# Kernel tuning notes

Hardware: AMD Instinct MI355X
Metric: run time of the kernel (lower is better)

Reference implementation:

```python
import jax, jax.numpy as jnp
import numpy as np

N, E, D, C = 50000, 800000, 96, 40
L2_EPS = 1e-12  # tf.nn.l2_normalize epsilon


def setup_inputs() -> dict:
    key = jax.random.key(0)
    ks = jax.random.split(key, 8)
    row = jnp.sort(jax.random.randint(ks[0], (E,), 0, N, dtype=jnp.int32))
    col = jax.random.randint(ks[1], (E,), 0, N, dtype=jnp.int32)
    vals = jax.random.uniform(ks[2], (E,), dtype=jnp.float32)
    x = jax.random.normal(ks[3], (N, D), dtype=jnp.float32)
    w1 = jax.random.normal(ks[4], (D, D), dtype=jnp.float32) * 0.1
    w2 = jax.random.normal(ks[5], (D, D), dtype=jnp.float32) * 0.1
    wc = jax.random.normal(ks[6], (D, C), dtype=jnp.float32) * 0.1
    bc = jnp.zeros((C,), dtype=jnp.float32)
    return {"row": row, "col": col, "vals": vals, "x": x,
            "w1": w1, "w2": w2, "wc": wc, "bc": bc}


def _spmm(row, col, vals, h):
    # sparse A (coo: row, col, vals) @ dense h, via gather + segment_sum
    msg = vals[:, None] * h[col]            # [E, D]
    return jax.ops.segment_sum(msg, row, num_segments=N)


def reference(row, col, vals, x, w1, w2, wc, bc):
    h = x
    for w in (w1, w2):                       # GCNConv: act(A @ (h @ W)), no bias
        h = jax.nn.relu(_spmm(row, col, vals, h @ w))
    # tf.nn.l2_normalize(h, axis=1)
    sq = jnp.sum(h * h, axis=1, keepdims=True)
    out = h * jax.lax.rsqrt(jnp.maximum(sq, L2_EPS))
    probs = jax.nn.softmax(out @ wc + bc, axis=-1)
    return out, probs
```

## Files before the change

### kernel.cpp

```cpp
#include <hip/hip_runtime.h>
#include <hip/hip_bf16.h>

#define GN 50000
#define GE 800000
#define GD 96
#define GC 40
#define L2EPS 1e-12f

typedef __attribute__((ext_vector_type(8))) short short8v;
typedef __attribute__((ext_vector_type(4))) float f32x4;

__device__ __forceinline__ unsigned f2bf(float x) {
    union { float f; unsigned u; } v; v.f = x;
    return (v.u + 0x7fffu + ((v.u >> 16) & 1u)) >> 16;
}
__device__ __forceinline__ float bflo(unsigned u) { return __uint_as_float(u << 16); }
__device__ __forceinline__ float bfhi(unsigned u) { return __uint_as_float(u & 0xffff0000u); }

__global__ void prep_k(const int* __restrict__ row, const float* __restrict__ w1,
                       const float* __restrict__ w2, int* __restrict__ rp,
                       unsigned* __restrict__ Wb1, unsigned* __restrict__ Wb2) {
    int i = blockIdx.x * blockDim.x + threadIdx.x;
    if (i <= GN) {
        int lo = 0, hi = GE;
        while (lo < hi) {
            int mid = (lo + hi) >> 1;
            if (row[mid] < i) lo = mid + 1; else hi = mid;
        }
        rp[i] = lo;
    }
    if (i < 2 * 4608) {
        const float* W = (i < 4608) ? w1 : w2;
        unsigned* Wb   = (i < 4608) ? Wb1 : Wb2;
        int j = (i < 4608) ? i : i - 4608;
        int r = j & 3;
        int lane = (j >> 2) & 63;
        int frag = j >> 8;
        int nt = frag / 3, kt = frag - nt * 3;
        int c = nt * 16 + (lane & 15);
        int k = kt * 32 + (lane >> 4) * 8 + r * 2;
        Wb[j] = f2bf(W[k * GD + c]) | (f2bf(W[(k + 1) * GD + c]) << 16);
    }
}

__global__ __launch_bounds__(64) void gemm_mfma_k(const float* __restrict__ A,
                                                  const uint4* __restrict__ Wb,
                                                  unsigned short* __restrict__ O) {
    const int tile = blockIdx.x;
    const int l  = threadIdx.x;
    const int m  = l & 15;
    const int kg = l >> 4;

    const float* arow = A + (size_t)(tile * 16 + m) * GD + kg * 8;
    short8v ah[3], al[3];
#pragma unroll
    for (int kt = 0; kt < 3; ++kt) {
        const float4* ap = reinterpret_cast<const float4*>(arow + kt * 32);
        float4 x0 = ap[0], x1 = ap[1];
        uint4 H, L;
        H.x = f2bf(x0.x) | (f2bf(x0.y) << 16);
        H.y = f2bf(x0.z) | (f2bf(x0.w) << 16);
        H.z = f2bf(x1.x) | (f2bf(x1.y) << 16);
        H.w = f2bf(x1.z) | (f2bf(x1.w) << 16);
        L.x = f2bf(x0.x - bflo(H.x)) | (f2bf(x0.y - bfhi(H.x)) << 16);
        L.y = f2bf(x0.z - bflo(H.y)) | (f2bf(x0.w - bfhi(H.y)) << 16);
        L.z = f2bf(x1.x - bflo(H.z)) | (f2bf(x1.y - bfhi(H.z)) << 16);
        L.w = f2bf(x1.z - bflo(H.w)) | (f2bf(x1.w - bfhi(H.w)) << 16);
        union { uint4 u; short8v s; } ch, cl;
        ch.u = H; cl.u = L;
        ah[kt] = ch.s; al[kt] = cl.s;
    }

#pragma unroll
    for (int nt = 0; nt < 6; ++nt) {
        f32x4 acc = {0.f, 0.f, 0.f, 0.f};
#pragma unroll
        for (int kt = 0; kt < 3; ++kt) {
            union { uint4 u; short8v s; } b;
            b.u = Wb[(nt * 3 + kt) * 64 + l];
            acc = __builtin_amdgcn_mfma_f32_16x16x32_bf16(ah[kt], b.s, acc, 0, 0, 0);
            acc = __builtin_amdgcn_mfma_f32_16x16x32_bf16(al[kt], b.s, acc, 0, 0, 0);
        }
        int ccol = nt * 16 + m;
#pragma unroll
        for (int reg = 0; reg < 4; ++reg) {
            int rrow = tile * 16 + kg * 4 + reg;
            O[(size_t)rrow * GD + ccol] = (unsigned short)f2bf(acc[reg]);
        }
    }
}

#define FMA8(U, V)                                                    \
    a0 += (V) * bflo((U).x); a1 += (V) * bfhi((U).x);                 \
    a2 += (V) * bflo((U).y); a3 += (V) * bfhi((U).y);                 \
    a4 += (V) * bflo((U).z); a5 += (V) * bfhi((U).z);                 \
    a6 += (V) * bflo((U).w); a7 += (V) * bfhi((U).w);

__global__ void spmm_relu_k(const int* __restrict__ rp, const int* __restrict__ col,
                            const float* __restrict__ vals,
                            const unsigned* __restrict__ Tb, float* __restrict__ H) {
    int idx = blockIdx.x * blockDim.x + threadIdx.x;
    int n = idx / 12;
    if (n >= GN) return;
    int t = idx - n * 12;
    int e0 = rp[n], e1 = rp[n + 1];
    float a0=0,a1=0,a2=0,a3=0,a4=0,a5=0,a6=0,a7=0;
    int e = e0;
    for (; e + 4 <= e1; e += 4) {
        int c0 = col[e], c1 = col[e+1], c2 = col[e+2], c3 = col[e+3];
        float v0 = vals[e], v1 = vals[e+1], v2 = vals[e+2], v3 = vals[e+3];
        uint4 u0 = *reinterpret_cast<const uint4*>(Tb + (size_t)c0 * 48 + t * 4);
        uint4 u1 = *reinterpret_cast<const uint4*>(Tb + (size_t)c1 * 48 + t * 4);
        uint4 u2 = *reinterpret_cast<const uint4*>(Tb + (size_t)c2 * 48 + t * 4);
        uint4 u3 = *reinterpret_cast<const uint4*>(Tb + (size_t)c3 * 48 + t * 4);
        FMA8(u0, v0) FMA8(u1, v1) FMA8(u2, v2) FMA8(u3, v3)
    }
    for (; e < e1; ++e) {
        float v = vals[e];
        uint4 u = *reinterpret_cast<const uint4*>(Tb + (size_t)col[e] * 48 + t * 4);
        FMA8(u, v)
    }
    float4* hr = reinterpret_cast<float4*>(H + (size_t)n * GD + t * 8);
    hr[0] = make_float4(fmaxf(a0,0.f), fmaxf(a1,0.f), fmaxf(a2,0.f), fmaxf(a3,0.f));
    hr[1] = make_float4(fmaxf(a4,0.f), fmaxf(a5,0.f), fmaxf(a6,0.f), fmaxf(a7,0.f));
}

#define FMA12(U, W_, V)                                               \
    a0 += (V) * bflo((U).x); a1 += (V) * bfhi((U).x);                 \
    a2 += (V) * bflo((U).y); a3 += (V) * bfhi((U).y);                 \
    a4 += (V) * bflo((U).z); a5 += (V) * bfhi((U).z);                 \
    a6 += (V) * bflo((U).w); a7 += (V) * bfhi((U).w);                 \
    a8 += (V) * bflo((W_).x); a9 += (V) * bfhi((W_).x);               \
    a10 += (V) * bflo((W_).y); a11 += (V) * bfhi((W_).y);

__global__ void spmm_relu_norm_k(const int* __restrict__ rp, const int* __restrict__ col,
                                 const float* __restrict__ vals,
                                 const unsigned* __restrict__ Tb, float* __restrict__ H) {
    int idx = blockIdx.x * blockDim.x + threadIdx.x;
    int n = idx >> 3;
    if (n >= GN) return;
    int t = idx & 7;
    int e0 = rp[n], e1 = rp[n + 1];
    float a0=0,a1=0,a2=0,a3=0,a4=0,a5=0,a6=0,a7=0,a8=0,a9=0,a10=0,a11=0;
    int e = e0;
    for (; e + 4 <= e1; e += 4) {
        int c0 = col[e], c1 = col[e+1], c2 = col[e+2], c3 = col[e+3];
        float v0 = vals[e], v1 = vals[e+1], v2 = vals[e+2], v3 = vals[e+3];
        const unsigned* r0p = Tb + (size_t)c0 * 48;
        const unsigned* r1p = Tb + (size_t)c1 * 48;
        const unsigned* r2p = Tb + (size_t)c2 * 48;
        const unsigned* r3p = Tb + (size_t)c3 * 48;
        uint4 u0 = *reinterpret_cast<const uint4*>(r0p + t * 4);
        uint2 w0 = *reinterpret_cast<const uint2*>(r0p + 32 + t * 2);
        uint4 u1 = *reinterpret_cast<const uint4*>(r1p + t * 4);
        uint2 w1 = *reinterpret_cast<const uint2*>(r1p + 32 + t * 2);
        uint4 u2 = *reinterpret_cast<const uint4*>(r2p + t * 4);
        uint2 w2 = *reinterpret_cast<const uint2*>(r2p + 32 + t * 2);
        uint4 u3 = *reinterpret_cast<const uint4*>(r3p + t * 4);
        uint2 w3 = *reinterpret_cast<const uint2*>(r3p + 32 + t * 2);
        FMA12(u0, w0, v0) FMA12(u1, w1, v1) FMA12(u2, w2, v2) FMA12(u3, w3, v3)
    }
    for (; e < e1; ++e) {
        float v = vals[e];
        const unsigned* r = Tb + (size_t)col[e] * 48;
        uint4 u = *reinterpret_cast<const uint4*>(r + t * 4);
        uint2 w = *reinterpret_cast<const uint2*>(r + 32 + t * 2);
        FMA12(u, w, v)
    }
    a0=fmaxf(a0,0.f); a1=fmaxf(a1,0.f); a2=fmaxf(a2,0.f); a3=fmaxf(a3,0.f);
    a4=fmaxf(a4,0.f); a5=fmaxf(a5,0.f); a6=fmaxf(a6,0.f); a7=fmaxf(a7,0.f);
    a8=fmaxf(a8,0.f); a9=fmaxf(a9,0.f); a10=fmaxf(a10,0.f); a11=fmaxf(a11,0.f);
    float ss = a0*a0+a1*a1+a2*a2+a3*a3+a4*a4+a5*a5+a6*a6+a7*a7+a8*a8+a9*a9+a10*a10+a11*a11;
    ss += __shfl_xor(ss, 1);
    ss += __shfl_xor(ss, 2);
    ss += __shfl_xor(ss, 4);
    float s = rsqrtf(fmaxf(ss, L2EPS));
    a0*=s; a1*=s; a2*=s; a3*=s; a4*=s; a5*=s;
    a6*=s; a7*=s; a8*=s; a9*=s; a10*=s; a11*=s;
    float4* hr = reinterpret_cast<float4*>(H + (size_t)n * GD + t * 8);
    hr[0] = make_float4(a0, a1, a2, a3);
    hr[1] = make_float4(a4, a5, a6, a7);
    *reinterpret_cast<float4*>(H + (size_t)n * GD + 64 + t * 4) =
        make_float4(a8, a9, a10, a11);
}

__global__ void cls_gemm_k(const float* __restrict__ A, const float* __restrict__ WC,
                           const float* __restrict__ BC, float* __restrict__ L) {
    __shared__ float4 w4[GD * 10];
    const float4* W4 = reinterpret_cast<const float4*>(WC);
    for (int i = threadIdx.x; i < GD * 10; i += blockDim.x) w4[i] = W4[i];
    __syncthreads();
    int idx = blockIdx.x * blockDim.x + threadIdx.x;
    if (idx >= (GN / 4) * 10) return;
    int rq = idx / 10;
    int q  = idx - rq * 10;
    int r0 = rq * 4;
    const float* a = A + (size_t)r0 * GD;
    float4 acc0 = {0,0,0,0}, acc1 = {0,0,0,0}, acc2 = {0,0,0,0}, acc3 = {0,0,0,0};
    for (int k0 = 0; k0 < GD; k0 += 4) {
        float4 a0 = *reinterpret_cast<const float4*>(a + k0);
        float4 a1 = *reinterpret_cast<const float4*>(a + GD + k0);
        float4 a2 = *reinterpret_cast<const float4*>(a + 2 * GD + k0);
        float4 a3 = *reinterpret_cast<const float4*>(a + 3 * GD + k0);
#pragma unroll
        for (int kk = 0; kk < 4; ++kk) {
            float4 w = w4[(k0 + kk) * 10 + q];
            float s0 = ((const float*)&a0)[kk];
            float s1 = ((const float*)&a1)[kk];
            float s2 = ((const float*)&a2)[kk];
            float s3 = ((const float*)&a3)[kk];
            acc0.x += s0 * w.x; acc0.y += s0 * w.y; acc0.z += s0 * w.z; acc0.w += s0 * w.w;
            acc1.x += s1 * w.x; acc1.y += s1 * w.y; acc1.z += s1 * w.z; acc1.w += s1 * w.w;
            acc2.x += s2 * w.x; acc2.y += s2 * w.y; acc2.z += s2 * w.z; acc2.w += s2 * w.w;
            acc3.x += s3 * w.x; acc3.y += s3 * w.y; acc3.z += s3 * w.z; acc3.w += s3 * w.w;
        }
    }
    float4 b = *reinterpret_cast<const float4*>(BC + q * 4);
    acc0.x += b.x; acc0.y += b.y; acc0.z += b.z; acc0.w += b.w;
    acc1.x += b.x; acc1.y += b.y; acc1.z += b.z; acc1.w += b.w;
    acc2.x += b.x; acc2.y += b.y; acc2.z += b.z; acc2.w += b.w;
    acc3.x += b.x; acc3.y += b.y; acc3.z += b.z; acc3.w += b.w;
    float4* L4 = reinterpret_cast<float4*>(L);
    L4[(size_t)(r0 + 0) * 10 + q] = acc0;
    L4[(size_t)(r0 + 1) * 10 + q] = acc1;
    L4[(size_t)(r0 + 2) * 10 + q] = acc2;
    L4[(size_t)(r0 + 3) * 10 + q] = acc3;
}

__global__ void softmax_k(const float* __restrict__ L, float* __restrict__ PROBS) {
    int n = blockIdx.x * blockDim.x + threadIdx.x;
    if (n >= GN) return;
    const float4* lr = reinterpret_cast<const float4*>(L + (size_t)n * GC);
    float4 v[10];
#pragma unroll
    for (int i = 0; i < 10; ++i) v[i] = lr[i];
    float m = -1e30f;
#pragma unroll
    for (int i = 0; i < 10; ++i)
        m = fmaxf(m, fmaxf(fmaxf(v[i].x, v[i].y), fmaxf(v[i].z, v[i].w)));
    float sum = 0.f;
#pragma unroll
    for (int i = 0; i < 10; ++i) {
        v[i].x = __expf(v[i].x - m); v[i].y = __expf(v[i].y - m);
        v[i].z = __expf(v[i].z - m); v[i].w = __expf(v[i].w - m);
        sum += v[i].x + v[i].y + v[i].z + v[i].w;
    }
    float inv = 1.f / sum;
    float4* pr = reinterpret_cast<float4*>(PROBS + (size_t)n * GC);
#pragma unroll
    for (int i = 0; i < 10; ++i) {
        v[i].x *= inv; v[i].y *= inv; v[i].z *= inv; v[i].w *= inv;
        pr[i] = v[i];
    }
}

extern "C" void kernel_launch(void* const* d_in, const int* in_sizes, int n_in,
                              void* d_out, int out_size, void* d_ws, size_t ws_size,
                              hipStream_t stream) {
    const int*   row  = (const int*)d_in[0];
    const int*   col  = (const int*)d_in[1];
    const float* vals = (const float*)d_in[2];
    const float* x    = (const float*)d_in[3];
    const float* w1   = (const float*)d_in[4];
    const float* w2   = (const float*)d_in[5];
    const float* wc   = (const float*)d_in[6];
    const float* bc   = (const float*)d_in[7];

    float* out   = (float*)d_out;
    float* probs = out + (size_t)GN * GD;

    char*  ws  = (char*)d_ws;
    int*   rp  = (int*)ws;
    size_t off = (((size_t)(GN + 1) * 4) + 511) & ~(size_t)511;
    unsigned* buf = (unsigned*)(ws + off);
    off += (size_t)GN * GD * 4;
    off = (off + 511) & ~(size_t)511;
    unsigned* Wb1 = (unsigned*)(ws + off);
    unsigned* Wb2 = Wb1 + 4608;

    prep_k<<<(GN + 1 + 255) / 256, 256, 0, stream>>>(row, w1, w2, rp, Wb1, Wb2);
    gemm_mfma_k<<<GN / 16, 64, 0, stream>>>(x, (const uint4*)Wb1, (unsigned short*)buf);
    spmm_relu_k<<<(GN * 12 + 255) / 256, 256, 0, stream>>>(rp, col, vals, buf, out);
    gemm_mfma_k<<<GN / 16, 64, 0, stream>>>(out, (const uint4*)Wb2, (unsigned short*)buf);
    spmm_relu_norm_k<<<(GN * 8 + 255) / 256, 256, 0, stream>>>(rp, col, vals, buf, out);
    cls_gemm_k<<<((GN / 4) * 10 + 255) / 256, 256, 0, stream>>>(out, wc, bc, (float*)buf);
    softmax_k<<<(GN + 255) / 256, 256, 0, stream>>>((float*)buf, probs);
}
```

Before: 108.9 us.

## Pack edges as (col,val) pairs reordered by column bucket per row

The prep kernel now builds an interleaved int2 edge array holding column and value. Within each row the edges are reordered into six column-range buckets, so gathers from the feature table are grouped by region for better cache locality. Both SpMM kernels read one 8-byte pair instead of two separate arrays, and the normalizing SpMM unroll drops from 4 to 2 edges. The cost is extra prep work per call (six passes per row plus more binary searches) and an additional 6.4 MB write.

```diff
diff --git a/kernel.cpp b/kernel.cpp
--- a/kernel.cpp
+++ b/kernel.cpp
@@ -6,6 +6,8 @@
 #define GD 96
 #define GC 40
 #define L2EPS 1e-12f
+#define NBUCKET 6
+#define BDIV 8334
 
 typedef __attribute__((ext_vector_type(8))) short short8v;
 typedef __attribute__((ext_vector_type(4))) float f32x4;
@@ -17,17 +19,31 @@
 __device__ __forceinline__ float bflo(unsigned u) { return __uint_as_float(u << 16); }
 __device__ __forceinline__ float bfhi(unsigned u) { return __uint_as_float(u & 0xffff0000u); }
 
-__global__ void prep_k(const int* __restrict__ row, const float* __restrict__ w1,
+__device__ __forceinline__ int lbound(const int* __restrict__ row, int key) {
+    int lo = 0, hi = GE;
+    while (lo < hi) {
+        int mid = (lo + hi) >> 1;
+        if (row[mid] < key) lo = mid + 1; else hi = mid;
+    }
+    return lo;
+}
+
+__global__ void prep_k(const int* __restrict__ row, const int* __restrict__ col,
+                       const float* __restrict__ vals, const float* __restrict__ w1,
                        const float* __restrict__ w2, int* __restrict__ rp,
-                       unsigned* __restrict__ Wb1, unsigned* __restrict__ Wb2) {
+                       int2* __restrict__ ep, unsigned* __restrict__ Wb1,
+                       unsigned* __restrict__ Wb2) {
     int i = blockIdx.x * blockDim.x + threadIdx.x;
-    if (i <= GN) {
-        int lo = 0, hi = GE;
-        while (lo < hi) {
-            int mid = (lo + hi) >> 1;
-            if (row[mid] < i) lo = mid + 1; else hi = mid;
-        }
-        rp[i] = lo;
+    if (i <= GN) rp[i] = lbound(row, i);
+    if (i < GN) {
+        int e0 = lbound(row, i);
+        int e1 = lbound(row, i + 1);
+        int w = e0;
+        for (int q = 0; q < NBUCKET; ++q)
+            for (int e = e0; e < e1; ++e) {
+                int c = col[e];
+                if (c / BDIV == q) ep[w++] = make_int2(c, __float_as_int(vals[e]));
+            }
     }
     if (i < 2 * 4608) {
         const float* W = (i < 4608) ? w1 : w2;
@@ -96,8 +112,7 @@
     a4 += (V) * bflo((U).z); a5 += (V) * bfhi((U).z);                 \
     a6 += (V) * bflo((U).w); a7 += (V) * bfhi((U).w);
 
-__global__ void spmm_relu_k(const int* __restrict__ rp, const int* __restrict__ col,
-                            const float* __restrict__ vals,
+__global__ void spmm_relu_k(const int* __restrict__ rp, const int2* __restrict__ ep,
                             const unsigned* __restrict__ Tb, float* __restrict__ H) {
     int idx = blockIdx.x * blockDim.x + threadIdx.x;
     int n = idx / 12;
@@ -107,18 +122,18 @@
     float a0=0,a1=0,a2=0,a3=0,a4=0,a5=0,a6=0,a7=0;
     int e = e0;
     for (; e + 4 <= e1; e += 4) {
-        int c0 = col[e], c1 = col[e+1], c2 = col[e+2], c3 = col[e+3];
-        float v0 = vals[e], v1 = vals[e+1], v2 = vals[e+2], v3 = vals[e+3];
-        uint4 u0 = *reinterpret_cast<const uint4*>(Tb + (size_t)c0 * 48 + t * 4);
-        uint4 u1 = *reinterpret_cast<const uint4*>(Tb + (size_t)c1 * 48 + t * 4);
-        uint4 u2 = *reinterpret_cast<const uint4*>(Tb + (size_t)c2 * 48 + t * 4);
-        uint4 u3 = *reinterpret_cast<const uint4*>(Tb + (size_t)c3 * 48 + t * 4);
-        FMA8(u0, v0) FMA8(u1, v1) FMA8(u2, v2) FMA8(u3, v3)
+        int2 p0 = ep[e], p1 = ep[e+1], p2 = ep[e+2], p3 = ep[e+3];
+        uint4 u0 = *reinterpret_cast<const uint4*>(Tb + (size_t)p0.x * 48 + t * 4);
+        uint4 u1 = *reinterpret_cast<const uint4*>(Tb + (size_t)p1.x * 48 + t * 4);
+        uint4 u2 = *reinterpret_cast<const uint4*>(Tb + (size_t)p2.x * 48 + t * 4);
+        uint4 u3 = *reinterpret_cast<const uint4*>(Tb + (size_t)p3.x * 48 + t * 4);
+        FMA8(u0, __int_as_float(p0.y)) FMA8(u1, __int_as_float(p1.y))
+        FMA8(u2, __int_as_float(p2.y)) FMA8(u3, __int_as_float(p3.y))
     }
     for (; e < e1; ++e) {
-        float v = vals[e];
-        uint4 u = *reinterpret_cast<const uint4*>(Tb + (size_t)col[e] * 48 + t * 4);
-        FMA8(u, v)
+        int2 p = ep[e];
+        uint4 u = *reinterpret_cast<const uint4*>(Tb + (size_t)p.x * 48 + t * 4);
+        FMA8(u, __int_as_float(p.y))
     }
     float4* hr = reinterpret_cast<float4*>(H + (size_t)n * GD + t * 8);
     hr[0] = make_float4(fmaxf(a0,0.f), fmaxf(a1,0.f), fmaxf(a2,0.f), fmaxf(a3,0.f));
@@ -133,8 +148,7 @@
     a8 += (V) * bflo((W_).x); a9 += (V) * bfhi((W_).x);               \
     a10 += (V) * bflo((W_).y); a11 += (V) * bfhi((W_).y);
 
-__global__ void spmm_relu_norm_k(const int* __restrict__ rp, const int* __restrict__ col,
-                                 const float* __restrict__ vals,
+__global__ void spmm_relu_norm_k(const int* __restrict__ rp, const int2* __restrict__ ep,
                                  const unsigned* __restrict__ Tb, float* __restrict__ H) {
     int idx = blockIdx.x * blockDim.x + threadIdx.x;
     int n = idx >> 3;
@@ -143,29 +157,22 @@
     int e0 = rp[n], e1 = rp[n + 1];
     float a0=0,a1=0,a2=0,a3=0,a4=0,a5=0,a6=0,a7=0,a8=0,a9=0,a10=0,a11=0;
     int e = e0;
-    for (; e + 4 <= e1; e += 4) {
-        int c0 = col[e], c1 = col[e+1], c2 = col[e+2], c3 = col[e+3];
-        float v0 = vals[e], v1 = vals[e+1], v2 = vals[e+2], v3 = vals[e+3];
-        const unsigned* r0p = Tb + (size_t)c0 * 48;
-        const unsigned* r1p = Tb + (size_t)c1 * 48;
-        const unsigned* r2p = Tb + (size_t)c2 * 48;
-        const unsigned* r3p = Tb + (size_t)c3 * 48;
+    for (; e + 2 <= e1; e += 2) {
+        int2 p0 = ep[e], p1 = ep[e+1];
+        const unsigned* r0p = Tb + (size_t)p0.x * 48;
+        const unsigned* r1p = Tb + (size_t)p1.x * 48;
         uint4 u0 = *reinterpret_cast<const uint4*>(r0p + t * 4);
         uint2 w0 = *reinterpret_cast<const uint2*>(r0p + 32 + t * 2);
         uint4 u1 = *reinterpret_cast<const uint4*>(r1p + t * 4);
         uint2 w1 = *reinterpret_cast<const uint2*>(r1p + 32 + t * 2);
-        uint4 u2 = *reinterpret_cast<const uint4*>(r2p + t * 4);
-        uint2 w2 = *reinterpret_cast<const uint2*>(r2p + 32 + t * 2);
-        uint4 u3 = *reinterpret_cast<const uint4*>(r3p + t * 4);
-        uint2 w3 = *reinterpret_cast<const uint2*>(r3p + 32 + t * 2);
-        FMA12(u0, w0, v0) FMA12(u1, w1, v1) FMA12(u2, w2, v2) FMA12(u3, w3, v3)
+        FMA12(u0, w0, __int_as_float(p0.y)) FMA12(u1, w1, __int_as_float(p1.y))
     }
     for (; e < e1; ++e) {
-        float v = vals[e];
-        const unsigned* r = Tb + (size_t)col[e] * 48;
+        int2 p = ep[e];
+        const unsigned* r = Tb + (size_t)p.x * 48;
         uint4 u = *reinterpret_cast<const uint4*>(r + t * 4);
         uint2 w = *reinterpret_cast<const uint2*>(r + 32 + t * 2);
-        FMA12(u, w, v)
+        FMA12(u, w, __int_as_float(p.y))
     }
     a0=fmaxf(a0,0.f); a1=fmaxf(a1,0.f); a2=fmaxf(a2,0.f); a3=fmaxf(a3,0.f);
     a4=fmaxf(a4,0.f); a5=fmaxf(a5,0.f); a6=fmaxf(a6,0.f); a7=fmaxf(a7,0.f);
@@ -275,14 +282,17 @@
     unsigned* buf = (unsigned*)(ws + off);
     off += (size_t)GN * GD * 4;
     off = (off + 511) & ~(size_t)511;
+    int2* ep   = (int2*)(ws + off);
+    off += (size_t)GE * 8;
+    off = (off + 511) & ~(size_t)511;
     unsigned* Wb1 = (unsigned*)(ws + off);
     unsigned* Wb2 = Wb1 + 4608;
 
-    prep_k<<<(GN + 1 + 255) / 256, 256, 0, stream>>>(row, w1, w2, rp, Wb1, Wb2);
+    prep_k<<<(GN + 1 + 255) / 256, 256, 0, stream>>>(row, col, vals, w1, w2, rp, ep, Wb1, Wb2);
     gemm_mfma_k<<<GN / 16, 64, 0, stream>>>(x, (const uint4*)Wb1, (unsigned short*)buf);
-    spmm_relu_k<<<(GN * 12 + 255) / 256, 256, 0, stream>>>(rp, col, vals, buf, out);
+    spmm_relu_k<<<(GN * 12 + 255) / 256, 256, 0, stream>>>(rp, ep, buf, out);
     gemm_mfma_k<<<GN / 16, 64, 0, stream>>>(out, (const uint4*)Wb2, (unsigned short*)buf);
-    spmm_relu_norm_k<<<(GN * 8 + 255) / 256, 256, 0, stream>>>(rp, col, vals, buf, out);
+    spmm_relu_norm_k<<<(GN * 8 + 255) / 256, 256, 0, stream>>>(rp, ep, buf, out);
     cls_gemm_k<<<((GN / 4) * 10 + 255) / 256, 256, 0, stream>>>(out, wc, bc, (float*)buf);
     softmax_k<<<(GN + 255) / 256, 256, 0, stream>>>((float*)buf, probs);
 }
```

New measurement: 150.1 us. +37.8%, slower.
